# Kernel optimization log

Hardware: AMD Instinct MI355X
Metric: run time of the kernel (lower is better)

The kernel has to match this reference:

```python
import jax, jax.numpy as jnp
import numpy as np

VOCAB = 20000
D = 512
B, S, C = 64, 256, 16


def setup_inputs() -> dict:
    key = jax.random.key(0)
    k1, k2, k3, k4, k5, k6, k7 = jax.random.split(key, 7)
    input_seqs = jax.random.randint(k1, (B, S, C), 0, VOCAB + 1)  # index VOCAB is padding row
    lengths = jax.random.randint(k2, (B,), 1, S + 1)
    scale = 1.0 / np.sqrt(D)
    emb_table = jax.random.normal(k3, (VOCAB + 1, D), dtype=jnp.float32)
    emb_table = emb_table.at[VOCAB].set(0.0)  # padding_idx row is zero
    w_ih = jax.random.uniform(k4, (4 * D, D), dtype=jnp.float32, minval=-scale, maxval=scale)
    w_hh = jax.random.uniform(k5, (4 * D, D), dtype=jnp.float32, minval=-scale, maxval=scale)
    w_out = jax.random.uniform(k6, (2, D), dtype=jnp.float32, minval=-scale, maxval=scale)
    b_out = jax.random.uniform(k7, (2,), dtype=jnp.float32, minval=-scale, maxval=scale)
    return {"input_seqs": input_seqs, "lengths": lengths, "emb_table": emb_table,
            "w_ih": w_ih, "w_hh": w_hh, "w_out": w_out, "b_out": b_out}


def reference(input_seqs, lengths, emb_table, w_ih, w_hh, w_out, b_out):
    # embedding lookup + sum over codes per visit: [B, S, D]
    table = emb_table.at[VOCAB].set(0.0)  # enforce zero padding row
    x = table[input_seqs].sum(axis=2)
    # dropout layers are identity at p=0.0 / eval
    xs = jnp.swapaxes(x, 0, 1)  # [S, B, D]

    def step(carry, xt):
        hx, cx = carry
        gates = xt @ w_ih.T + hx @ w_hh.T  # [B, 4D], no bias
        i, f, g, o = jnp.split(gates, 4, axis=-1)  # torch LSTMCell gate order: i, f, g, o
        i = jax.nn.sigmoid(i)
        f = jax.nn.sigmoid(f)
        g = jnp.tanh(g)
        o = jax.nn.sigmoid(o)
        cx = f * cx + i * g
        hx = o * jnp.tanh(cx)
        return (hx, cx), hx

    h0 = jnp.zeros((x.shape[0], D), dtype=x.dtype)
    c0 = jnp.zeros((x.shape[0], D), dtype=x.dtype)
    _, hiddens = jax.lax.scan(step, (h0, c0), xs)  # [S, B, D]
    hiddens = jnp.swapaxes(hiddens, 0, 1)  # [B, S, D]
    final_hidden = hiddens[jnp.arange(x.shape[0]), lengths - 1]  # [B, D]
    out = final_hidden @ w_out.T + b_out  # [B, 2]
    return out
```

## Files before the change

kernel.cpp:

```cpp
#include <hip/hip_runtime.h>
#include <hip/hip_fp16.h>

typedef _Float16 f16;
typedef __attribute__((ext_vector_type(8))) _Float16 f16x8;
typedef __attribute__((ext_vector_type(4))) _Float16 f16x4;
typedef __attribute__((ext_vector_type(4))) float f32x4;

#define D_      512
#define NG_     2048
#define B_      64
#define S_      256
#define C_      16
#define M_      (B_*S_)

#define OFF_X    0ull
#define SZ_X     ((unsigned long long)M_*D_*2)
#define OFF_G    (OFF_X + SZ_X)
#define SZ_G     ((unsigned long long)M_*NG_*2)
#define OFF_WI   (OFF_G + SZ_G)
#define SZ_WI    ((unsigned long long)NG_*D_*2)
#define OFF_HG   (OFF_WI + SZ_WI)
#define SZ_HG    (2ull*4*16*512*2)
#define OFF_FH   (OFF_HG + SZ_HG)
#define SZ_FH    ((unsigned long long)B_*D_*4)
#define OFF_FL   (OFF_FH + SZ_FH)
#define SZ_FL    1024ull
#define WS_NEED  (OFF_FL + SZ_FL)

__device__ __forceinline__ float sigmoidf_(float x) { return 1.f / (1.f + __expf(-x)); }
__device__ __forceinline__ float tanhf_(float x) {
  float a = fabsf(x);
  float e = __expf(-2.f * a);
  float r = (1.f - e) / (1.f + e);
  return copysignf(r, x);
}

__global__ void k_zero(unsigned* __restrict__ p) { p[threadIdx.x] = 0u; }

__global__ void k_embed(const int* __restrict__ seqs, const float* __restrict__ table,
                        f16* __restrict__ x) {
  const int m = blockIdx.x;
  const int t = threadIdx.x;
  const int* idx = seqs + (size_t)m * C_;
  float4 acc = {0.f, 0.f, 0.f, 0.f};
  #pragma unroll
  for (int r = 0; r < C_; ++r) {
    int id = idx[r];
    const float4* row = (const float4*)(table + (size_t)id * D_);
    float4 v = row[t];
    acc.x += v.x; acc.y += v.y; acc.z += v.z; acc.w += v.w;
  }
  f16x4 o;
  o[0] = (f16)acc.x; o[1] = (f16)acc.y; o[2] = (f16)acc.z; o[3] = (f16)acc.w;
  *(f16x4*)(x + (size_t)m * D_ + t * 4) = o;
}

__global__ void k_cvtw(const float* __restrict__ w, f16* __restrict__ o, int n) {
  int i = blockIdx.x * 256 + threadIdx.x;
  if (i < n) o[i] = (f16)w[i];
}

__global__ void k_gemm_ih(const f16* __restrict__ x, const f16* __restrict__ wi,
                          f16* __restrict__ G) {
  const int mt = blockIdx.x, nt = blockIdx.y;
  const int wid = threadIdx.x >> 6, lane = threadIdx.x & 63;
  const int lr = lane & 15, lq = lane >> 4;
  const int m0 = mt * 64 + wid * 16;
  const int n0 = nt * 64;

  f32x4 acc[4] = {{0.f,0.f,0.f,0.f},{0.f,0.f,0.f,0.f},{0.f,0.f,0.f,0.f},{0.f,0.f,0.f,0.f}};
  for (int kt = 0; kt < 16; ++kt) {
    const int k0 = kt * 32 + lq * 8;
    const f16x8 a = *(const f16x8*)(x + (size_t)(m0 + lr) * D_ + k0);
    #pragma unroll
    for (int j = 0; j < 4; ++j) {
      const f16x8 b = *(const f16x8*)(wi + (size_t)(n0 + j * 16 + lr) * D_ + k0);
      acc[j] = __builtin_amdgcn_mfma_f32_16x16x32_f16(a, b, acc[j], 0, 0, 0);
    }
  }
  #pragma unroll
  for (int j = 0; j < 4; ++j)
    #pragma unroll
    for (int rr = 0; rr < 4; ++rr) {
      const int m = m0 + lq * 4 + rr;
      const int n = n0 + j * 16 + lr;
      G[(size_t)m * NG_ + n] = (f16)acc[j][rr];
    }
}

__global__ __launch_bounds__(512, 1) void k_lstm(
    const float* __restrict__ whh, const f16* __restrict__ G,
    const int* __restrict__ lengths, unsigned* __restrict__ hGu,
    unsigned* __restrict__ flags, float* __restrict__ final_h) {
  const int bid = blockIdx.x;
  const int cl = bid & 3;
  const int r = bid >> 2;
  const int tid = threadIdx.x;
  const int wid = tid >> 6, lane = tid & 63;
  const int lr = lane & 15, lq = lane >> 4;

  __shared__ f16 h_lds[16][520];
  __shared__ float glds[4][32][20];
  __shared__ int steps_sh;

  const int gi = wid >> 1, jh = wid & 1;
  const int nrow = gi * 512 + r * 32 + jh * 16 + lr;
  f16x8 wfrag[16];
  #pragma unroll
  for (int kt = 0; kt < 16; ++kt) {
    const int k0 = kt * 32 + lq * 8;
    const float* p = whh + (size_t)nrow * D_ + k0;
    f16x8 w;
    #pragma unroll
    for (int e = 0; e < 8; ++e) w[e] = (f16)p[e];
    wfrag[kt] = w;
  }

  for (int i = tid; i < 16 * 520; i += 512) ((f16*)h_lds)[i] = (f16)0.f;

  const int ec = tid >> 5;
  const int ej = tid & 31;
  const int b_ec = cl * 16 + ec;
  const int len_ec = lengths[b_ec];

  if (tid == 0) {
    int mx = 0;
    for (int c = 0; c < 16; ++c) mx = max(mx, lengths[cl * 16 + c]);
    steps_sh = mx;
  }
  float cstate = 0.f;
  __syncthreads();
  const int steps = steps_sh;

  unsigned* flag = flags + cl * 64;
  const f16* Gbase = G + (size_t)(cl * 16) * S_ * NG_;

  for (int t = 0; t < steps; ++t) {
    f32x4 acc = {0.f, 0.f, 0.f, 0.f};
    #pragma unroll
    for (int kt = 0; kt < 16; ++kt) {
      const f16x8 a = *(const f16x8*)&h_lds[lr][kt * 32 + lq * 8];
      acc = __builtin_amdgcn_mfma_f32_16x16x32_f16(a, wfrag[kt], acc, 0, 0, 0);
    }
    *(f32x4*)&glds[gi][jh * 16 + lr][lq * 4] = acc;
    __syncthreads();

    {
      const f16* gp = Gbase + (size_t)(ec * S_ + t) * NG_ + r * 32 + ej;
      float ig = glds[0][ej][ec] + (float)gp[0];
      float fg = glds[1][ej][ec] + (float)gp[512];
      float gg = glds[2][ej][ec] + (float)gp[1024];
      float og = glds[3][ej][ec] + (float)gp[1536];
      ig = sigmoidf_(ig); fg = sigmoidf_(fg); og = sigmoidf_(og); gg = tanhf_(gg);
      cstate = fg * cstate + ig * gg;
      const float hv = og * tanhf_(cstate);
      if (t == len_ec - 1) final_h[(size_t)b_ec * D_ + r * 32 + ej] = hv;

      unsigned hb = (unsigned)(unsigned short)__builtin_bit_cast(unsigned short, (f16)hv);
      unsigned other = __shfl_xor(hb, 1);
      if (!(ej & 1)) {
        unsigned packed = hb | (other << 16);
        const int buf = t & 1;
        __hip_atomic_store(&hGu[(size_t)buf * 4096 * 4 + cl * 4096 + ec * 256 + r * 16 + (ej >> 1)],
                           packed, __ATOMIC_RELAXED, __HIP_MEMORY_SCOPE_AGENT);
      }
    }
    __syncthreads();

    if (tid == 0) {
      __hip_atomic_fetch_add(flag, 1u, __ATOMIC_RELEASE, __HIP_MEMORY_SCOPE_AGENT);
      const unsigned target = (unsigned)(t + 1) * 16u;
      while (__hip_atomic_load(flag, __ATOMIC_ACQUIRE, __HIP_MEMORY_SCOPE_AGENT) < target) {
        __builtin_amdgcn_s_sleep(1);
      }
    }
    __syncthreads();

    {
      const int buf = t & 1;
      const size_t base = (size_t)buf * 4096 * 4 + cl * 4096 + tid * 8;
      unsigned v[8];
      #pragma unroll
      for (int e = 0; e < 8; ++e)
        v[e] = __hip_atomic_load(&hGu[base + e], __ATOMIC_RELAXED, __HIP_MEMORY_SCOPE_AGENT);
      const int c = tid >> 5, k0 = (tid & 31) * 16;
      unsigned* dst = (unsigned*)&h_lds[c][k0];
      #pragma unroll
      for (int e = 0; e < 8; ++e) dst[e] = v[e];
    }
    __syncthreads();
  }
}

__global__ void k_head(const float* __restrict__ fh, const float* __restrict__ wout,
                       const float* __restrict__ bout, float* __restrict__ out) {
  const int b = blockIdx.x;
  const int lane = threadIdx.x;
  float p0 = 0.f, p1 = 0.f;
  for (int k = lane; k < D_; k += 64) {
    const float h = fh[(size_t)b * D_ + k];
    p0 += h * wout[k];
    p1 += h * wout[D_ + k];
  }
  #pragma unroll
  for (int off = 32; off; off >>= 1) {
    p0 += __shfl_down(p0, off);
    p1 += __shfl_down(p1, off);
  }
  if (lane == 0) {
    out[b * 2 + 0] = p0 + bout[0];
    out[b * 2 + 1] = p1 + bout[1];
  }
}

extern "C" void kernel_launch(void* const* d_in, const int* in_sizes, int n_in,
                              void* d_out, int out_size, void* d_ws, size_t ws_size,
                              hipStream_t stream) {
  const int* seqs = (const int*)d_in[0];
  const int* lengths = (const int*)d_in[1];
  const float* table = (const float*)d_in[2];
  const float* wih = (const float*)d_in[3];
  const float* whh = (const float*)d_in[4];
  const float* wout = (const float*)d_in[5];
  const float* bout = (const float*)d_in[6];
  float* out = (float*)d_out;
  char* ws = (char*)d_ws;
  if (ws_size < WS_NEED) return;

  f16* x = (f16*)(ws + OFF_X);
  f16* G = (f16*)(ws + OFF_G);
  f16* wi16 = (f16*)(ws + OFF_WI);
  unsigned* hGu = (unsigned*)(ws + OFF_HG);
  float* fh = (float*)(ws + OFF_FH);
  unsigned* flags = (unsigned*)(ws + OFF_FL);

  hipLaunchKernelGGL(k_zero, dim3(1), dim3(256), 0, stream, flags);
  hipLaunchKernelGGL(k_embed, dim3(M_), dim3(128), 0, stream, seqs, table, x);
  hipLaunchKernelGGL(k_cvtw, dim3((NG_ * D_ + 255) / 256), dim3(256), 0, stream,
                     wih, wi16, NG_ * D_);
  hipLaunchKernelGGL(k_gemm_ih, dim3(M_ / 64, NG_ / 64), dim3(256), 0, stream, x, wi16, G);
  hipLaunchKernelGGL(k_lstm, dim3(64), dim3(512), 0, stream, whh, G, lengths, hGu, flags, fh);
  hipLaunchKernelGGL(k_head, dim3(B_), dim3(64), 0, stream, fh, wout, bout, out);
}
```

Before: 1.682 ms.

## Halve LSTM workgroups, interleave gate columns, and replace atomic barrier with per-block flags

The recurrent kernel now runs on 32 workgroups, each owning 64 hidden columns with two MFMA accumulators per wave and two batch rows per thread. The cross-block barrier's atomic counter plus single-thread spin is replaced by per-workgroup sequence flags; each thread polls only the producer flag it needs. The input-gate GEMM writes gates interleaved so one f16x4 load fetches all four gates, and the next step's values are prefetched during the current step. The aim is lower per-step synchronisation and memory latency, at the cost of more register pressure and fewer CUs doing the recurrent work.

```diff
diff --git a/kernel.cpp b/kernel.cpp
--- a/kernel.cpp
+++ b/kernel.cpp
@@ -20,11 +20,11 @@
 #define OFF_WI   (OFF_G + SZ_G)
 #define SZ_WI    ((unsigned long long)NG_*D_*2)
 #define OFF_HG   (OFF_WI + SZ_WI)
-#define SZ_HG    (2ull*4*16*512*2)
+#define SZ_HG    (2ull*4*16*256*4)
 #define OFF_FH   (OFF_HG + SZ_HG)
 #define SZ_FH    ((unsigned long long)B_*D_*4)
 #define OFF_FL   (OFF_FH + SZ_FH)
-#define SZ_FL    1024ull
+#define SZ_FL    (32ull*64*4)
 #define WS_NEED  (OFF_FL + SZ_FL)
 
 __device__ __forceinline__ float sigmoidf_(float x) { return 1.f / (1.f + __expf(-x)); }
@@ -35,7 +35,9 @@
   return copysignf(r, x);
 }
 
-__global__ void k_zero(unsigned* __restrict__ p) { p[threadIdx.x] = 0u; }
+__global__ void k_zero(unsigned* __restrict__ p) {
+  for (int i = threadIdx.x; i < 32 * 64; i += 256) p[i] = 0u;
+}
 
 __global__ void k_embed(const int* __restrict__ seqs, const float* __restrict__ table,
                         f16* __restrict__ x) {
@@ -61,12 +63,14 @@
 }
 
 __global__ void k_gemm_ih(const f16* __restrict__ x, const f16* __restrict__ wi,
-                          f16* __restrict__ G) {
-  const int mt = blockIdx.x, nt = blockIdx.y;
+                          f16* __restrict__ G2) {
+  const int nt = blockIdx.x, mt = blockIdx.y;
   const int wid = threadIdx.x >> 6, lane = threadIdx.x & 63;
   const int lr = lane & 15, lq = lane >> 4;
   const int m0 = mt * 64 + wid * 16;
   const int n0 = nt * 64;
+  const int gate = nt >> 3;
+  const int cbase = (nt & 7) * 64;
 
   f32x4 acc[4] = {{0.f,0.f,0.f,0.f},{0.f,0.f,0.f,0.f},{0.f,0.f,0.f,0.f},{0.f,0.f,0.f,0.f}};
   for (int kt = 0; kt < 16; ++kt) {
@@ -83,15 +87,15 @@
     #pragma unroll
     for (int rr = 0; rr < 4; ++rr) {
       const int m = m0 + lq * 4 + rr;
-      const int n = n0 + j * 16 + lr;
-      G[(size_t)m * NG_ + n] = (f16)acc[j][rr];
+      const int col = cbase + j * 16 + lr;
+      G2[(size_t)m * NG_ + col * 4 + gate] = (f16)acc[j][rr];
     }
 }
 
 __global__ __launch_bounds__(512, 1) void k_lstm(
-    const float* __restrict__ whh, const f16* __restrict__ G,
+    const float* __restrict__ whh, const f16* __restrict__ G2,
     const int* __restrict__ lengths, unsigned* __restrict__ hGu,
-    unsigned* __restrict__ flags, float* __restrict__ final_h) {
+    unsigned* __restrict__ seq, float* __restrict__ final_h) {
   const int bid = blockIdx.x;
   const int cl = bid & 3;
   const int r = bid >> 2;
@@ -99,92 +103,123 @@
   const int wid = tid >> 6, lane = tid & 63;
   const int lr = lane & 15, lq = lane >> 4;
 
-  __shared__ f16 h_lds[16][520];
-  __shared__ float glds[4][32][20];
+  __shared__ f16 h_lds[16][522];
+  __shared__ float glds[4][64][21];
   __shared__ int steps_sh;
 
-  const int gi = wid >> 1, jh = wid & 1;
-  const int nrow = gi * 512 + r * 32 + jh * 16 + lr;
-  f16x8 wfrag[16];
-  #pragma unroll
-  for (int kt = 0; kt < 16; ++kt) {
-    const int k0 = kt * 32 + lq * 8;
-    const float* p = whh + (size_t)nrow * D_ + k0;
-    f16x8 w;
-    #pragma unroll
-    for (int e = 0; e < 8; ++e) w[e] = (f16)p[e];
-    wfrag[kt] = w;
-  }
-
-  for (int i = tid; i < 16 * 520; i += 512) ((f16*)h_lds)[i] = (f16)0.f;
-
-  const int ec = tid >> 5;
-  const int ej = tid & 31;
-  const int b_ec = cl * 16 + ec;
-  const int len_ec = lengths[b_ec];
+  f16x8 wf0[16], wf1[16];
+  {
+    const int nl0 = wid * 32 + lr;
+    const int nl1 = nl0 + 16;
+    const int row0 = (nl0 >> 6) * 512 + r * 64 + (nl0 & 63);
+    const int row1 = (nl1 >> 6) * 512 + r * 64 + (nl1 & 63);
+    for (int kt = 0; kt < 16; ++kt) {
+      const int k0 = kt * 32 + lq * 8;
+      const float* p0 = whh + (size_t)row0 * D_ + k0;
+      const float* p1 = whh + (size_t)row1 * D_ + k0;
+      f16x8 w0, w1;
+      #pragma unroll
+      for (int e = 0; e < 8; ++e) { w0[e] = (f16)p0[e]; w1[e] = (f16)p1[e]; }
+      wf0[kt] = w0; wf1[kt] = w1;
+    }
+  }
+  for (int i = tid; i < 16 * 522; i += 512) ((f16*)h_lds)[i] = (f16)0.f;
+
+  const int ej = lane;
+  const int ec0 = wid;
+  const int b0 = cl * 16 + ec0, b1 = b0 + 8;
+  const int len0 = lengths[b0], len1 = lengths[b1];
 
   if (tid == 0) {
     int mx = 0;
     for (int c = 0; c < 16; ++c) mx = max(mx, lengths[cl * 16 + c]);
     steps_sh = mx;
   }
-  float cstate = 0.f;
+  float cs0 = 0.f, cs1 = 0.f;
   __syncthreads();
   const int steps = steps_sh;
 
-  unsigned* flag = flags + cl * 64;
-  const f16* Gbase = G + (size_t)(cl * 16) * S_ * NG_;
+  const int gc = tid & 15;
+  const int gq = tid >> 4;
+  unsigned* pollflag = seq + (cl * 8 + (gq >> 2)) * 64;
+  unsigned* wgflag = seq + (cl * 8 + r) * 64;
+
+  const size_t gb0 = (size_t)b0 * S_ * NG_ + (r * 64 + ej) * 4;
+  const size_t gb1 = (size_t)b1 * S_ * NG_ + (r * 64 + ej) * 4;
+  f16x4 gfa = *(const f16x4*)(G2 + gb0);
+  f16x4 gfb = *(const f16x4*)(G2 + gb1);
 
   for (int t = 0; t < steps; ++t) {
-    f32x4 acc = {0.f, 0.f, 0.f, 0.f};
+    f32x4 acc0 = {0.f,0.f,0.f,0.f}, acc1 = {0.f,0.f,0.f,0.f};
     #pragma unroll
     for (int kt = 0; kt < 16; ++kt) {
       const f16x8 a = *(const f16x8*)&h_lds[lr][kt * 32 + lq * 8];
-      acc = __builtin_amdgcn_mfma_f32_16x16x32_f16(a, wfrag[kt], acc, 0, 0, 0);
-    }
-    *(f32x4*)&glds[gi][jh * 16 + lr][lq * 4] = acc;
+      acc0 = __builtin_amdgcn_mfma_f32_16x16x32_f16(a, wf0[kt], acc0, 0, 0, 0);
+      acc1 = __builtin_amdgcn_mfma_f32_16x16x32_f16(a, wf1[kt], acc1, 0, 0, 0);
+    }
+    {
+      const int nl0 = wid * 32 + lr, nl1 = nl0 + 16;
+      #pragma unroll
+      for (int rr = 0; rr < 4; ++rr) {
+        glds[nl0 >> 6][nl0 & 63][lq * 4 + rr] = acc0[rr];
+        glds[nl1 >> 6][nl1 & 63][lq * 4 + rr] = acc1[rr];
+      }
+    }
     __syncthreads();
 
     {
-      const f16* gp = Gbase + (size_t)(ec * S_ + t) * NG_ + r * 32 + ej;
-      float ig = glds[0][ej][ec] + (float)gp[0];
-      float fg = glds[1][ej][ec] + (float)gp[512];
-      float gg = glds[2][ej][ec] + (float)gp[1024];
-      float og = glds[3][ej][ec] + (float)gp[1536];
+      float ig = glds[0][ej][ec0] + (float)gfa[0];
+      float fg = glds[1][ej][ec0] + (float)gfa[1];
+      float gg = glds[2][ej][ec0] + (float)gfa[2];
+      float og = glds[3][ej][ec0] + (float)gfa[3];
       ig = sigmoidf_(ig); fg = sigmoidf_(fg); og = sigmoidf_(og); gg = tanhf_(gg);
-      cstate = fg * cstate + ig * gg;
-      const float hv = og * tanhf_(cstate);
-      if (t == len_ec - 1) final_h[(size_t)b_ec * D_ + r * 32 + ej] = hv;
-
-      unsigned hb = (unsigned)(unsigned short)__builtin_bit_cast(unsigned short, (f16)hv);
-      unsigned other = __shfl_xor(hb, 1);
+      cs0 = fg * cs0 + ig * gg;
+      const float hv0 = og * tanhf_(cs0);
+      if (t == len0 - 1) final_h[(size_t)b0 * D_ + r * 64 + ej] = hv0;
+
+      float ig1 = glds[0][ej][ec0 + 8] + (float)gfb[0];
+      float fg1 = glds[1][ej][ec0 + 8] + (float)gfb[1];
+      float gg1 = glds[2][ej][ec0 + 8] + (float)gfb[2];
+      float og1 = glds[3][ej][ec0 + 8] + (float)gfb[3];
+      ig1 = sigmoidf_(ig1); fg1 = sigmoidf_(fg1); og1 = sigmoidf_(og1); gg1 = tanhf_(gg1);
+      cs1 = fg1 * cs1 + ig1 * gg1;
+      const float hv1 = og1 * tanhf_(cs1);
+      if (t == len1 - 1) final_h[(size_t)b1 * D_ + r * 64 + ej] = hv1;
+
+      unsigned h0 = (unsigned)(unsigned short)__builtin_bit_cast(unsigned short, (f16)hv0);
+      unsigned h1 = (unsigned)(unsigned short)__builtin_bit_cast(unsigned short, (f16)hv1);
+      unsigned o0 = __shfl_xor(h0, 1);
+      unsigned o1 = __shfl_xor(h1, 1);
       if (!(ej & 1)) {
-        unsigned packed = hb | (other << 16);
-        const int buf = t & 1;
-        __hip_atomic_store(&hGu[(size_t)buf * 4096 * 4 + cl * 4096 + ec * 256 + r * 16 + (ej >> 1)],
-                           packed, __ATOMIC_RELAXED, __HIP_MEMORY_SCOPE_AGENT);
+        const size_t sb = (size_t)(t & 1) * 16384 + cl * 4096;
+        const int kp = r * 32 + (ej >> 1);
+        __hip_atomic_store(&hGu[sb + ec0 * 256 + kp],
+                           h0 | (o0 << 16), __ATOMIC_RELAXED, __HIP_MEMORY_SCOPE_AGENT);
+        __hip_atomic_store(&hGu[sb + (ec0 + 8) * 256 + kp],
+                           h1 | (o1 << 16), __ATOMIC_RELAXED, __HIP_MEMORY_SCOPE_AGENT);
       }
     }
+
+    {
+      const int tn = min(t + 1, S_ - 1);
+      gfa = *(const f16x4*)(G2 + gb0 + (size_t)tn * NG_);
+      gfb = *(const f16x4*)(G2 + gb1 + (size_t)tn * NG_);
+    }
     __syncthreads();
 
-    if (tid == 0) {
-      __hip_atomic_fetch_add(flag, 1u, __ATOMIC_RELEASE, __HIP_MEMORY_SCOPE_AGENT);
-      const unsigned target = (unsigned)(t + 1) * 16u;
-      while (__hip_atomic_load(flag, __ATOMIC_ACQUIRE, __HIP_MEMORY_SCOPE_AGENT) < target) {
-        __builtin_amdgcn_s_sleep(1);
-      }
-    }
-    __syncthreads();
-
-    {
-      const int buf = t & 1;
-      const size_t base = (size_t)buf * 4096 * 4 + cl * 4096 + tid * 8;
+    if (tid == 0)
+      __hip_atomic_store(wgflag, (unsigned)(t + 1), __ATOMIC_RELEASE, __HIP_MEMORY_SCOPE_AGENT);
+
+    while (__hip_atomic_load(pollflag, __ATOMIC_ACQUIRE, __HIP_MEMORY_SCOPE_AGENT)
+           < (unsigned)(t + 1))
+      __builtin_amdgcn_s_sleep(1);
+    {
+      const size_t base = (size_t)(t & 1) * 16384 + cl * 4096 + gc * 256 + gq * 8;
       unsigned v[8];
       #pragma unroll
       for (int e = 0; e < 8; ++e)
         v[e] = __hip_atomic_load(&hGu[base + e], __ATOMIC_RELAXED, __HIP_MEMORY_SCOPE_AGENT);
-      const int c = tid >> 5, k0 = (tid & 31) * 16;
-      unsigned* dst = (unsigned*)&h_lds[c][k0];
+      unsigned* dst = (unsigned*)&h_lds[gc][gq * 16];
       #pragma unroll
       for (int e = 0; e < 8; ++e) dst[e] = v[e];
     }
@@ -228,17 +263,17 @@
   if (ws_size < WS_NEED) return;
 
   f16* x = (f16*)(ws + OFF_X);
-  f16* G = (f16*)(ws + OFF_G);
+  f16* G2 = (f16*)(ws + OFF_G);
   f16* wi16 = (f16*)(ws + OFF_WI);
   unsigned* hGu = (unsigned*)(ws + OFF_HG);
   float* fh = (float*)(ws + OFF_FH);
-  unsigned* flags = (unsigned*)(ws + OFF_FL);
-
-  hipLaunchKernelGGL(k_zero, dim3(1), dim3(256), 0, stream, flags);
+  unsigned* seqf = (unsigned*)(ws + OFF_FL);
+
+  hipLaunchKernelGGL(k_zero, dim3(1), dim3(256), 0, stream, seqf);
   hipLaunchKernelGGL(k_embed, dim3(M_), dim3(128), 0, stream, seqs, table, x);
   hipLaunchKernelGGL(k_cvtw, dim3((NG_ * D_ + 255) / 256), dim3(256), 0, stream,
                      wih, wi16, NG_ * D_);
-  hipLaunchKernelGGL(k_gemm_ih, dim3(M_ / 64, NG_ / 64), dim3(256), 0, stream, x, wi16, G);
-  hipLaunchKernelGGL(k_lstm, dim3(64), dim3(512), 0, stream, whh, G, lengths, hGu, flags, fh);
+  hipLaunchKernelGGL(k_gemm_ih, dim3(NG_ / 64, M_ / 64), dim3(256), 0, stream, x, wi16, G2);
+  hipLaunchKernelGGL(k_lstm, dim3(32), dim3(512), 0, stream, whh, G2, lengths, hGu, seqf, fh);
   hipLaunchKernelGGL(k_head, dim3(B_), dim3(64), 0, stream, fh, wout, bout, out);
 }
```

New measurement: 2.196 ms. +30.5%, slower.

## Replace per-cluster barrier counter with per-workgroup step flags and prefetch interleaved gates

Applied to the files above, without the earlier changes.

The shared atomic counter plus thread-0 spin is replaced by per-workgroup sequence flags. Each wave waits only on the two producer workgroups whose hidden-state slices it reads, which removes one block-wide barrier per step. The input-gate GEMM now writes gates interleaved as [col][4], so each thread loads one 8-byte vector for the next step, prefetched during the current one. LDS strides are padded to reduce bank conflicts, and the GEMM grid order is swapped. The risk is more polling traffic on flags, and the unvectorized glds stores add some instructions.

```diff
diff --git a/kernel.cpp b/kernel.cpp
--- a/kernel.cpp
+++ b/kernel.cpp
@@ -20,11 +20,11 @@
 #define OFF_WI   (OFF_G + SZ_G)
 #define SZ_WI    ((unsigned long long)NG_*D_*2)
 #define OFF_HG   (OFF_WI + SZ_WI)
-#define SZ_HG    (2ull*4*16*512*2)
+#define SZ_HG    (2ull*4*16*256*4)
 #define OFF_FH   (OFF_HG + SZ_HG)
 #define SZ_FH    ((unsigned long long)B_*D_*4)
 #define OFF_FL   (OFF_FH + SZ_FH)
-#define SZ_FL    1024ull
+#define SZ_FL    (64ull*64*4)
 #define WS_NEED  (OFF_FL + SZ_FL)
 
 __device__ __forceinline__ float sigmoidf_(float x) { return 1.f / (1.f + __expf(-x)); }
@@ -35,7 +35,9 @@
   return copysignf(r, x);
 }
 
-__global__ void k_zero(unsigned* __restrict__ p) { p[threadIdx.x] = 0u; }
+__global__ void k_zero(unsigned* __restrict__ p) {
+  for (int i = threadIdx.x; i < 64 * 64; i += 256) p[i] = 0u;
+}
 
 __global__ void k_embed(const int* __restrict__ seqs, const float* __restrict__ table,
                         f16* __restrict__ x) {
@@ -61,12 +63,14 @@
 }
 
 __global__ void k_gemm_ih(const f16* __restrict__ x, const f16* __restrict__ wi,
-                          f16* __restrict__ G) {
-  const int mt = blockIdx.x, nt = blockIdx.y;
+                          f16* __restrict__ G2) {
+  const int nt = blockIdx.x, mt = blockIdx.y;
   const int wid = threadIdx.x >> 6, lane = threadIdx.x & 63;
   const int lr = lane & 15, lq = lane >> 4;
   const int m0 = mt * 64 + wid * 16;
   const int n0 = nt * 64;
+  const int gate = nt >> 3;
+  const int cbase = (nt & 7) * 64;
 
   f32x4 acc[4] = {{0.f,0.f,0.f,0.f},{0.f,0.f,0.f,0.f},{0.f,0.f,0.f,0.f},{0.f,0.f,0.f,0.f}};
   for (int kt = 0; kt < 16; ++kt) {
@@ -83,15 +87,15 @@
     #pragma unroll
     for (int rr = 0; rr < 4; ++rr) {
       const int m = m0 + lq * 4 + rr;
-      const int n = n0 + j * 16 + lr;
-      G[(size_t)m * NG_ + n] = (f16)acc[j][rr];
+      const int col = cbase + j * 16 + lr;
+      G2[(size_t)m * NG_ + col * 4 + gate] = (f16)acc[j][rr];
     }
 }
 
 __global__ __launch_bounds__(512, 1) void k_lstm(
-    const float* __restrict__ whh, const f16* __restrict__ G,
+    const float* __restrict__ whh, const f16* __restrict__ G2,
     const int* __restrict__ lengths, unsigned* __restrict__ hGu,
-    unsigned* __restrict__ flags, float* __restrict__ final_h) {
+    unsigned* __restrict__ seq, float* __restrict__ final_h) {
   const int bid = blockIdx.x;
   const int cl = bid & 3;
   const int r = bid >> 2;
@@ -99,8 +103,8 @@
   const int wid = tid >> 6, lane = tid & 63;
   const int lr = lane & 15, lq = lane >> 4;
 
-  __shared__ f16 h_lds[16][520];
-  __shared__ float glds[4][32][20];
+  __shared__ f16 h_lds[16][522];
+  __shared__ float glds[4][32][21];
   __shared__ int steps_sh;
 
   const int gi = wid >> 1, jh = wid & 1;
@@ -116,7 +120,7 @@
     wfrag[kt] = w;
   }
 
-  for (int i = tid; i < 16 * 520; i += 512) ((f16*)h_lds)[i] = (f16)0.f;
+  for (int i = tid; i < 16 * 522; i += 512) ((f16*)h_lds)[i] = (f16)0.f;
 
   const int ec = tid >> 5;
   const int ej = tid & 31;
@@ -132,8 +136,14 @@
   __syncthreads();
   const int steps = steps_sh;
 
-  unsigned* flag = flags + cl * 64;
-  const f16* Gbase = G + (size_t)(cl * 16) * S_ * NG_;
+  const int gc = tid & 15;
+  const int gq = tid >> 4;
+  unsigned* flagA = seq + (cl * 16 + 2 * wid) * 64;
+  unsigned* flagB = flagA + 64;
+  unsigned* wgflag = seq + (cl * 16 + r) * 64;
+
+  const size_t gb = (size_t)b_ec * S_ * NG_ + (size_t)(r * 32 + ej) * 4;
+  f16x4 gf = *(const f16x4*)(G2 + gb);
 
   for (int t = 0; t < steps; ++t) {
     f32x4 acc = {0.f, 0.f, 0.f, 0.f};
@@ -142,15 +152,16 @@
       const f16x8 a = *(const f16x8*)&h_lds[lr][kt * 32 + lq * 8];
       acc = __builtin_amdgcn_mfma_f32_16x16x32_f16(a, wfrag[kt], acc, 0, 0, 0);
     }
-    *(f32x4*)&glds[gi][jh * 16 + lr][lq * 4] = acc;
+    #pragma unroll
+    for (int rr = 0; rr < 4; ++rr)
+      glds[gi][jh * 16 + lr][lq * 4 + rr] = acc[rr];
     __syncthreads();
 
     {
-      const f16* gp = Gbase + (size_t)(ec * S_ + t) * NG_ + r * 32 + ej;
-      float ig = glds[0][ej][ec] + (float)gp[0];
-      float fg = glds[1][ej][ec] + (float)gp[512];
-      float gg = glds[2][ej][ec] + (float)gp[1024];
-      float og = glds[3][ej][ec] + (float)gp[1536];
+      float ig = glds[0][ej][ec] + (float)gf[0];
+      float fg = glds[1][ej][ec] + (float)gf[1];
+      float gg = glds[2][ej][ec] + (float)gf[2];
+      float og = glds[3][ej][ec] + (float)gf[3];
       ig = sigmoidf_(ig); fg = sigmoidf_(fg); og = sigmoidf_(og); gg = tanhf_(gg);
       cstate = fg * cstate + ig * gg;
       const float hv = og * tanhf_(cstate);
@@ -159,32 +170,34 @@
       unsigned hb = (unsigned)(unsigned short)__builtin_bit_cast(unsigned short, (f16)hv);
       unsigned other = __shfl_xor(hb, 1);
       if (!(ej & 1)) {
-        unsigned packed = hb | (other << 16);
-        const int buf = t & 1;
-        __hip_atomic_store(&hGu[(size_t)buf * 4096 * 4 + cl * 4096 + ec * 256 + r * 16 + (ej >> 1)],
-                           packed, __ATOMIC_RELAXED, __HIP_MEMORY_SCOPE_AGENT);
+        const size_t sb = (size_t)(t & 1) * 16384 + cl * 4096;
+        __hip_atomic_store(&hGu[sb + ec * 256 + r * 16 + (ej >> 1)],
+                           hb | (other << 16), __ATOMIC_RELAXED, __HIP_MEMORY_SCOPE_AGENT);
       }
     }
+
+    {
+      const int tn = min(t + 1, S_ - 1);
+      gf = *(const f16x4*)(G2 + gb + (size_t)tn * NG_);
+    }
     __syncthreads();
 
-    if (tid == 0) {
-      __hip_atomic_fetch_add(flag, 1u, __ATOMIC_RELEASE, __HIP_MEMORY_SCOPE_AGENT);
-      const unsigned target = (unsigned)(t + 1) * 16u;
-      while (__hip_atomic_load(flag, __ATOMIC_ACQUIRE, __HIP_MEMORY_SCOPE_AGENT) < target) {
-        __builtin_amdgcn_s_sleep(1);
-      }
-    }
-    __syncthreads();
-
+    if (tid == 0)
+      __hip_atomic_store(wgflag, (unsigned)(t + 1), __ATOMIC_RELEASE, __HIP_MEMORY_SCOPE_AGENT);
+
+    while (__hip_atomic_load(flagA, __ATOMIC_ACQUIRE, __HIP_MEMORY_SCOPE_AGENT)
+           < (unsigned)(t + 1))
+      __builtin_amdgcn_s_sleep(1);
+    while (__hip_atomic_load(flagB, __ATOMIC_ACQUIRE, __HIP_MEMORY_SCOPE_AGENT)
+           < (unsigned)(t + 1))
+      __builtin_amdgcn_s_sleep(1);
     {
-      const int buf = t & 1;
-      const size_t base = (size_t)buf * 4096 * 4 + cl * 4096 + tid * 8;
+      const size_t base = (size_t)(t & 1) * 16384 + cl * 4096 + gc * 256 + gq * 8;
       unsigned v[8];
       #pragma unroll
       for (int e = 0; e < 8; ++e)
         v[e] = __hip_atomic_load(&hGu[base + e], __ATOMIC_RELAXED, __HIP_MEMORY_SCOPE_AGENT);
-      const int c = tid >> 5, k0 = (tid & 31) * 16;
-      unsigned* dst = (unsigned*)&h_lds[c][k0];
+      unsigned* dst = (unsigned*)&h_lds[gc][gq * 16];
       #pragma unroll
       for (int e = 0; e < 8; ++e) dst[e] = v[e];
     }
@@ -228,17 +241,17 @@
   if (ws_size < WS_NEED) return;
 
   f16* x = (f16*)(ws + OFF_X);
-  f16* G = (f16*)(ws + OFF_G);
+  f16* G2 = (f16*)(ws + OFF_G);
   f16* wi16 = (f16*)(ws + OFF_WI);
   unsigned* hGu = (unsigned*)(ws + OFF_HG);
   float* fh = (float*)(ws + OFF_FH);
-  unsigned* flags = (unsigned*)(ws + OFF_FL);
-
-  hipLaunchKernelGGL(k_zero, dim3(1), dim3(256), 0, stream, flags);
+  unsigned* seqf = (unsigned*)(ws + OFF_FL);
+
+  hipLaunchKernelGGL(k_zero, dim3(1), dim3(256), 0, stream, seqf);
   hipLaunchKernelGGL(k_embed, dim3(M_), dim3(128), 0, stream, seqs, table, x);
   hipLaunchKernelGGL(k_cvtw, dim3((NG_ * D_ + 255) / 256), dim3(256), 0, stream,
                      wih, wi16, NG_ * D_);
-  hipLaunchKernelGGL(k_gemm_ih, dim3(M_ / 64, NG_ / 64), dim3(256), 0, stream, x, wi16, G);
-  hipLaunchKernelGGL(k_lstm, dim3(64), dim3(512), 0, stream, whh, G, lengths, hGu, flags, fh);
+  hipLaunchKernelGGL(k_gemm_ih, dim3(NG_ / 64, M_ / 64), dim3(256), 0, stream, x, wi16, G2);
+  hipLaunchKernelGGL(k_lstm, dim3(64), dim3(512), 0, stream, whh, G2, lengths, hGu, seqf, fh);
   hipLaunchKernelGGL(k_head, dim3(B_), dim3(64), 0, stream, fh, wout, bout, out);
 }
```

Result: slower. 3.720 ms (+121.1%).
